# Performance work log

Measured on AMD Instinct MI355X. Metric: run time of the kernel, lower is better.

Reference implementation:

```python
import jax, jax.numpy as jnp
import numpy as np

K = 3            # kernel_size
FILTERS = 256
GC = 16          # group_channels (hardcoded in module)
G = FILTERS // GC  # groups = 16


def setup_inputs() -> dict:
    key = jax.random.key(0)
    ks = jax.random.split(key, 5)
    B, H, W, C = 8, 64, 64, FILTERS
    red = FILTERS // 4  # reduction_ratio = 4
    x = jax.random.normal(ks[0], (B, H, W, C), dtype=jnp.float32)
    W1 = jax.random.normal(ks[1], (C, red), dtype=jnp.float32) * 0.05
    b1 = jnp.zeros((red,), dtype=jnp.float32)
    W2 = jax.random.normal(ks[2], (red, K * K * G), dtype=jnp.float32) * 0.05
    b2 = jnp.zeros((K * K * G,), dtype=jnp.float32)
    return {"x": x, "W1": W1, "b1": b1, "W2": W2, "b2": b2}


def reference(x, W1, b1, W2, b2):
    b, h, w, c = x.shape
    kk = K * K
    # kernel generator: two 1x1 convs (note: norm1/relu1 are defined but unused in the original call())
    wgt = jnp.einsum('bhwc,cd->bhwd', x, W1) + b1          # [b,h,w,c/4]
    wgt = jnp.einsum('bhwd,de->bhwe', wgt, W2) + b2        # [b,h,w,kk*G]
    # transpose to channel-first, reshape (b, G, kk, h, w), expand group-channel dim
    wgt = wgt.transpose(0, 3, 1, 2).reshape(b, G, 1, kk, h, w)
    # SAME-padded 3x3 patch extraction, stride 1; TF depth layout is (ki, kj, c)
    pad = (K - 1) // 2
    xp = jnp.pad(x, ((0, 0), (pad, K - 1 - pad), (pad, K - 1 - pad), (0, 0)))
    patches = jnp.stack([xp[:, i:i + h, j:j + w, :] for i in range(K) for j in range(K)], axis=3)  # [b,h,w,kk,c]
    # replicate TF's transpose + row-major reshape of the (kk*c) flat dim into (G, GC, kk)
    out = patches.reshape(b, h, w, kk * c).transpose(0, 3, 1, 2).reshape(b, G, GC, kk, h, w)
    out = jnp.einsum('bgokhw,bgckhw->bgchw', wgt, out)     # multiply + reduce over kk
    out = out.reshape(b, FILTERS, h, w).transpose(0, 2, 3, 1)
    return out
```

## Files before the change

### kernel.cpp

```cpp
#include <hip/hip_runtime.h>

namespace {
constexpr int XP = 264;
constexpr int XR = 18 * XP;
constexpr int EWP = 148;

typedef _Float16 h2 __attribute__((ext_vector_type(2)));
typedef _Float16 h8 __attribute__((ext_vector_type(8)));
typedef float f32x4 __attribute__((ext_vector_type(4)));

__device__ __forceinline__ h2 pkrtz(float a, float b) {
  return __builtin_bit_cast(h2, __builtin_amdgcn_cvt_pkrtz(a, b));
}

#if __has_builtin(__builtin_amdgcn_fdot2)
#define HAS_FDOT2 1
#else
#define HAS_FDOT2 0
#endif

__global__ __launch_bounds__(256) void prep_w12(
    const float* __restrict__ W1, const float* __restrict__ b1,
    const float* __restrict__ W2, const float* __restrict__ b2,
    _Float16* __restrict__ pack, float* __restrict__ b12)
{
  const int t = threadIdx.x;
  const int T = blockIdx.x;
  if (T < 9) {
    __shared__ float sw2[64 * 16];
    for (int i = t; i < 1024; i += 256) {
      int d = i >> 4, n = i & 15;
      sw2[i] = W2[d * 144 + T * 16 + n];
    }
    __syncthreads();
    const int c = t;
    float acc[16];
#pragma unroll
    for (int n = 0; n < 16; ++n) acc[n] = 0.f;
    for (int d = 0; d < 64; d += 4) {
      float4 w1 = *(const float4*)(W1 + c * 64 + d);
#pragma unroll
      for (int dd = 0; dd < 4; ++dd) {
        float a = (dd == 0) ? w1.x : (dd == 1) ? w1.y : (dd == 2) ? w1.z : w1.w;
        const float* r = &sw2[(d + dd) * 16];
#pragma unroll
        for (int n = 0; n < 16; ++n) acc[n] += a * r[n];
      }
    }
    int s = c >> 5, q = (c >> 3) & 3, j = c & 7;
#pragma unroll
    for (int n = 0; n < 16; ++n)
      pack[(((T * 8 + s) * 64 + q * 16 + n) << 3) + j] = (_Float16)acc[n];
  } else if (t < 144) {
    float bb = b2[t];
    for (int d = 0; d < 64; ++d) bb += b1[d] * W2[d * 144 + t];
    b12[t] = bb;
  }
}

__global__ __launch_bounds__(256) void invo_fused(
    const float* __restrict__ x,
    const _Float16* __restrict__ pack,
    const float* __restrict__ b12g,
    float* __restrict__ out)
{
  __shared__ __align__(16) _Float16 xg[3 * XR];
  __shared__ float ew[16 * EWP];

  const int t = threadIdx.x;
  const int blk = blockIdx.x;
  const int b = blk & 7;
  const int r_ = blk >> 3;
  const int strip = r_ & 3;
  const int h = r_ >> 2;
  const int w0 = strip * 16;
  const int pix0 = ((b << 6) + h) * 64 + w0;

  for (int idx = t; idx < 3 * 18 * 64; idx += 256) {
    int c4 = (idx & 63) << 2;
    int pr = idx >> 6;
    int r = (pr >= 36) ? 2 : (pr >= 18 ? 1 : 0);
    int j = pr - r * 18;
    int hh = h + r - 1, ww = w0 + j - 1;
    float4 v = make_float4(0.f, 0.f, 0.f, 0.f);
    if (((unsigned)hh < 64u) && ((unsigned)ww < 64u))
      v = *(const float4*)(x + ((((b << 6) + hh) << 6) + ww) * 256 + c4);
    h2 lo = pkrtz(v.x, v.y), hi = pkrtz(v.z, v.w);
    uint2 u;
    u.x = __builtin_bit_cast(unsigned, lo);
    u.y = __builtin_bit_cast(unsigned, hi);
    *(uint2*)(&xg[r * XR + j * XP + c4]) = u;
  }
  __syncthreads();

  {
    const int wave = t >> 6, lane = t & 63;
    const int q = lane >> 4, m = lane & 15;
    h8 A[8];
    const _Float16* arow = &xg[XR + (m + 1) * XP + q * 8];
#pragma unroll
    for (int s = 0; s < 8; ++s)
      A[s] = *(const h8*)(arow + s * 32);
    for (int T = wave; T < 9; T += 4) {
      f32x4 acc = {0.f, 0.f, 0.f, 0.f};
      const h8* bp = (const h8*)pack + (T * 8) * 64 + lane;
#pragma unroll
      for (int s = 0; s < 8; ++s)
        acc = __builtin_amdgcn_mfma_f32_16x16x32_f16(A[s], bp[s * 64], acc, 0, 0, 0);
      float bb = b12g[T * 16 + m];
#pragma unroll
      for (int r = 0; r < 4; ++r)
        ew[(q * 4 + r) * EWP + T * 16 + m] = acc[r] + bb;
    }
  }
  __syncthreads();

  {
    const int p = t >> 4, g = t & 15;
    float ewr[9];
#pragma unroll
    for (int k = 0; k < 9; ++k) ewr[k] = ew[p * EWP + g * 9 + k];
    h2 wp[8];
#pragma unroll
    for (int m = 0; m < 8; ++m)
      wp[m] = pkrtz(ewr[m], ewr[m + 1]);
    const float w8 = ewr[8], wb0 = ewr[0];
    const int g144 = g * 144;
    const int pbase = p * XP;
    float res[16];
#pragma unroll
    for (int gc = 0; gc < 16; ++gc) res[gc] = 0.f;
#pragma unroll
    for (int j = 0; j < 18; ++j) {
      int f = g144 + j * 8;
      int tap = f >> 8;
      int ch = f & 255;
      int di = (tap * 86) >> 8;
      int dj = tap - 3 * di;
      uint4 dv = *(const uint4*)(&xg[di * XR + (p + dj) * XP + ch]);
      h2 v[4];
      v[0] = __builtin_bit_cast(h2, dv.x);
      v[1] = __builtin_bit_cast(h2, dv.y);
      v[2] = __builtin_bit_cast(h2, dv.z);
      v[3] = __builtin_bit_cast(h2, dv.w);
#pragma unroll
      for (int i = 0; i < 4; ++i) {
        const int u = j * 8 + 2 * i;
        const int m = u % 9;
        if (m == 8) {
          res[u / 9]     += (float)v[i][0] * w8;
          res[u / 9 + 1] += (float)v[i][1] * wb0;
        } else {
#if HAS_FDOT2
          res[u / 9] = __builtin_amdgcn_fdot2(v[i], wp[m], res[u / 9], false);
#else
          res[u / 9] += (float)v[i][0] * ewr[m] + (float)v[i][1] * ewr[m + 1];
#endif
        }
      }
    }
    float* orow = out + (size_t)(pix0 + p) * 256 + (g << 4);
    *(float4*)(orow + 0)  = make_float4(res[0],  res[1],  res[2],  res[3]);
    *(float4*)(orow + 4)  = make_float4(res[4],  res[5],  res[6],  res[7]);
    *(float4*)(orow + 8)  = make_float4(res[8],  res[9],  res[10], res[11]);
    *(float4*)(orow + 12) = make_float4(res[12], res[13], res[14], res[15]);
  }
}
}

extern "C" void kernel_launch(void* const* d_in, const int* in_sizes, int n_in,
                              void* d_out, int out_size, void* d_ws, size_t ws_size,
                              hipStream_t stream) {
  const float* x  = (const float*)d_in[0];
  const float* W1 = (const float*)d_in[1];
  const float* b1 = (const float*)d_in[2];
  const float* W2 = (const float*)d_in[3];
  const float* b2 = (const float*)d_in[4];
  float* out = (float*)d_out;
  _Float16* pack = (_Float16*)d_ws;
  float* b12 = (float*)((char*)d_ws + 73728);
  prep_w12<<<10, 256, 0, stream>>>(W1, b1, W2, b2, pack, b12);
  invo_fused<<<2048, 256, 0, stream>>>(x, pack, b12, out);
}
```

Measured before the change: 114.5 us.

## Pre-pack padded fp16 input slabs and load tiles via global-to-LDS DMA

Adds a prep kernel that converts x to fp16 and writes zero-padded 18-wide strip slabs into workspace. The main kernel then fills shared memory with direct global_load_lds 16-byte transfers, so it no longer needs per-element bounds checks and fp32-to-fp16 conversion in the load loop. In exchange it makes an extra full pass over x, with writes to and reads from a workspace buffer, plus an extra kernel launch. It falls back to the old kernel if the workspace is too small.

```diff
diff --git a/kernel.cpp b/kernel.cpp
--- a/kernel.cpp
+++ b/kernel.cpp
@@ -4,6 +4,7 @@
 constexpr int XP = 264;
 constexpr int XR = 18 * XP;
 constexpr int EWP = 148;
+constexpr size_t SLAB = (size_t)67 * XR;
 
 typedef _Float16 h2 __attribute__((ext_vector_type(2)));
 typedef _Float16 h8 __attribute__((ext_vector_type(8)));
@@ -11,6 +12,12 @@
 
 __device__ __forceinline__ h2 pkrtz(float a, float b) {
   return __builtin_bit_cast(h2, __builtin_amdgcn_cvt_pkrtz(a, b));
+}
+
+__device__ __forceinline__ void load_lds16(const void* g, void* l) {
+  __builtin_amdgcn_global_load_lds(
+      (const __attribute__((address_space(1))) void*)g,
+      (__attribute__((address_space(3))) void*)l, 16, 0, 0);
 }
 
 #if __has_builtin(__builtin_amdgcn_fdot2)
@@ -58,13 +65,42 @@
   }
 }
 
-__global__ __launch_bounds__(256) void invo_fused(
-    const float* __restrict__ x,
+__global__ __launch_bounds__(256) void prep_xpad(
+    const float* __restrict__ x, _Float16* __restrict__ xpad)
+{
+  const int t = threadIdx.x;
+  const int blk = blockIdx.x;
+  const int s = blk % 66;
+  const int bs = blk / 66;
+  const int b = bs >> 2, strip = bs & 3;
+  const int w0 = strip * 16;
+  const int hsrc = s - 1;
+  const bool rowok = (unsigned)hsrc < 64u;
+  _Float16* dst0 = xpad + (SLAB * bs) + (size_t)s * XR;
+  for (int idx = t; idx < 594; idx += 256) {
+    int j = idx / 33, cc = idx % 33;
+    int w = w0 + j - 1;
+    uint4 o = make_uint4(0u, 0u, 0u, 0u);
+    if (rowok && cc < 32 && (unsigned)w < 64u) {
+      const float* src = x + (((size_t)(b * 64 + hsrc) * 64 + w) << 8) + cc * 8;
+      float4 v0 = *(const float4*)(src);
+      float4 v1 = *(const float4*)(src + 4);
+      o.x = __builtin_bit_cast(unsigned, pkrtz(v0.x, v0.y));
+      o.y = __builtin_bit_cast(unsigned, pkrtz(v0.z, v0.w));
+      o.z = __builtin_bit_cast(unsigned, pkrtz(v1.x, v1.y));
+      o.w = __builtin_bit_cast(unsigned, pkrtz(v1.z, v1.w));
+    }
+    *(uint4*)(dst0 + j * XP + cc * 8) = o;
+  }
+}
+
+__global__ __launch_bounds__(256) void invo_fused_dma(
+    const _Float16* __restrict__ xpad,
     const _Float16* __restrict__ pack,
     const float* __restrict__ b12g,
     float* __restrict__ out)
 {
-  __shared__ __align__(16) _Float16 xg[3 * XR];
+  __shared__ __align__(16) _Float16 xg[1792 * 8];
   __shared__ float ew[16 * EWP];
 
   const int t = threadIdx.x;
@@ -75,7 +111,107 @@
   const int h = r_ >> 2;
   const int w0 = strip * 16;
   const int pix0 = ((b << 6) + h) * 64 + w0;
-
+  const int wave = t >> 6, lane = t & 63;
+
+  {
+    const char* gsrc = (const char*)(xpad + SLAB * (b * 4 + strip) + (size_t)h * XR);
+    char* lds = (char*)xg;
+    const int base = wave * 7168 + lane * 16;
+#pragma unroll
+    for (int i = 0; i < 7; ++i) {
+      int off = base + i * 1024;
+      load_lds16(gsrc + off, lds + off);
+    }
+  }
+  __syncthreads();
+
+  {
+    const int q = lane >> 4, m = lane & 15;
+    h8 A[8];
+    const _Float16* arow = &xg[XR + (m + 1) * XP + q * 8];
+#pragma unroll
+    for (int s = 0; s < 8; ++s)
+      A[s] = *(const h8*)(arow + s * 32);
+    for (int T = wave; T < 9; T += 4) {
+      f32x4 acc = {0.f, 0.f, 0.f, 0.f};
+      const h8* bp = (const h8*)pack + (T * 8) * 64 + lane;
+#pragma unroll
+      for (int s = 0; s < 8; ++s)
+        acc = __builtin_amdgcn_mfma_f32_16x16x32_f16(A[s], bp[s * 64], acc, 0, 0, 0);
+      float bb = b12g[T * 16 + m];
+#pragma unroll
+      for (int r = 0; r < 4; ++r)
+        ew[(q * 4 + r) * EWP + T * 16 + m] = acc[r] + bb;
+    }
+  }
+  __syncthreads();
+
+  {
+    const int p = t >> 4, g = t & 15;
+    float ewr[9];
+#pragma unroll
+    for (int k = 0; k < 9; ++k) ewr[k] = ew[p * EWP + g * 9 + k];
+    h2 wp[8];
+#pragma unroll
+    for (int m = 0; m < 8; ++m)
+      wp[m] = pkrtz(ewr[m], ewr[m + 1]);
+    const float w8 = ewr[8], wb0 = ewr[0];
+    const int g144 = g * 144;
+    const int pbase = p * XP;
+    float res[16];
+#pragma unroll
+    for (int gc = 0; gc < 16; ++gc) res[gc] = 0.f;
+#pragma unroll
+    for (int j = 0; j < 18; ++j) {
+      int f = g144 + j * 8;
+      int tap = f >> 8;
+      int ch = f & 255;
+      int di = (tap * 86) >> 8;
+      int dj = tap - 3 * di;
+      uint4 dv = *(const uint4*)(&xg[di * XR + (p + dj) * XP + ch]);
+      h2 v[4];
+      v[0] = __builtin_bit_cast(h2, dv.x);
+      v[1] = __builtin_bit_cast(h2, dv.y);
+      v[2] = __builtin_bit_cast(h2, dv.z);
+      v[3] = __builtin_bit_cast(h2, dv.w);
+#pragma unroll
+      for (int i = 0; i < 4; ++i) {
+        const int u = j * 8 + 2 * i;
+        const int m = u % 9;
+        if (m == 8) {
+          res[u / 9]     += (float)v[i][0] * w8;
+          res[u / 9 + 1] += (float)v[i][1] * wb0;
+        } else {
+#if HAS_FDOT2
+          res[u / 9] = __builtin_amdgcn_fdot2(v[i], wp[m], res[u / 9], false);
+#else
+          res[u / 9] += (float)v[i][0] * ewr[m] + (float)v[i][1] * ewr[m + 1];
+#endif
+        }
+      }
+    }
+    float* orow = out + (size_t)(pix0 + p) * 256 + (g << 4);
+    *(float4*)(orow + 0)  = make_float4(res[0],  res[1],  res[2],  res[3]);
+    *(float4*)(orow + 4)  = make_float4(res[4],  res[5],  res[6],  res[7]);
+    *(float4*)(orow + 8)  = make_float4(res[8],  res[9],  res[10], res[11]);
+    *(float4*)(orow + 12) = make_float4(res[12], res[13], res[14], res[15]);
+  }
+}
+
+__global__ __launch_bounds__(256) void invo_fused(
+    const float* __restrict__ x, const _Float16* __restrict__ pack,
+    const float* __restrict__ b12g, float* __restrict__ out)
+{
+  __shared__ __align__(16) _Float16 xg[3 * XR];
+  __shared__ float ew[16 * EWP];
+  const int t = threadIdx.x;
+  const int blk = blockIdx.x;
+  const int b = blk & 7;
+  const int r_ = blk >> 3;
+  const int strip = r_ & 3;
+  const int h = r_ >> 2;
+  const int w0 = strip * 16;
+  const int pix0 = ((b << 6) + h) * 64 + w0;
   for (int idx = t; idx < 3 * 18 * 64; idx += 256) {
     int c4 = (idx & 63) << 2;
     int pr = idx >> 6;
@@ -92,15 +228,13 @@
     *(uint2*)(&xg[r * XR + j * XP + c4]) = u;
   }
   __syncthreads();
-
   {
     const int wave = t >> 6, lane = t & 63;
     const int q = lane >> 4, m = lane & 15;
     h8 A[8];
     const _Float16* arow = &xg[XR + (m + 1) * XP + q * 8];
 #pragma unroll
-    for (int s = 0; s < 8; ++s)
-      A[s] = *(const h8*)(arow + s * 32);
+    for (int s = 0; s < 8; ++s) A[s] = *(const h8*)(arow + s * 32);
     for (int T = wave; T < 9; T += 4) {
       f32x4 acc = {0.f, 0.f, 0.f, 0.f};
       const h8* bp = (const h8*)pack + (T * 8) * 64 + lane;
@@ -114,7 +248,6 @@
     }
   }
   __syncthreads();
-
   {
     const int p = t >> 4, g = t & 15;
     float ewr[9];
@@ -122,8 +255,7 @@
     for (int k = 0; k < 9; ++k) ewr[k] = ew[p * EWP + g * 9 + k];
     h2 wp[8];
 #pragma unroll
-    for (int m = 0; m < 8; ++m)
-      wp[m] = pkrtz(ewr[m], ewr[m + 1]);
+    for (int m = 0; m < 8; ++m) wp[m] = pkrtz(ewr[m], ewr[m + 1]);
     const float w8 = ewr[8], wb0 = ewr[0];
     const int g144 = g * 144;
     const int pbase = p * XP;
@@ -179,6 +311,13 @@
   float* out = (float*)d_out;
   _Float16* pack = (_Float16*)d_ws;
   float* b12 = (float*)((char*)d_ws + 73728);
+  _Float16* xpad = (_Float16*)((char*)d_ws + 131072);
+  const size_t ENEED = 131072 + (size_t)32 * SLAB * 2;
   prep_w12<<<10, 256, 0, stream>>>(W1, b1, W2, b2, pack, b12);
-  invo_fused<<<2048, 256, 0, stream>>>(x, pack, b12, out);
-}
+  if (ws_size >= ENEED) {
+    prep_xpad<<<8 * 4 * 66, 256, 0, stream>>>(x, xpad);
+    invo_fused_dma<<<2048, 256, 0, stream>>>(xpad, pack, b12, out);
+  } else {
+    invo_fused<<<2048, 256, 0, stream>>>(x, pack, b12, out);
+  }
+}
```

New measurement: 116.9 us. +2.2%, slower.

## Widen fused involution tile to 32 pixels with 512-thread blocks

Applied to the files above, without the earlier changes.

Each block now processes a 32-pixel strip instead of 16 and runs 512 threads. This cuts the halo overhead of staging the 3-row input tile in shared memory, since the block loads 34 columns for 32 outputs rather than 18 for 16. The global loads are batched into explicit register arrays so more of them are in flight before conversion to fp16, and the first weight tile for the MFMA stage is prefetched before the barrier. In exchange, shared memory per block roughly doubles, which may reduce the number of resident blocks per CU.

```diff
diff --git a/kernel.cpp b/kernel.cpp
--- a/kernel.cpp
+++ b/kernel.cpp
@@ -2,7 +2,7 @@
 
 namespace {
 constexpr int XP = 264;
-constexpr int XR = 18 * XP;
+constexpr int XRr = 34 * XP;
 constexpr int EWP = 148;
 
 typedef _Float16 h2 __attribute__((ext_vector_type(2)));
@@ -58,50 +58,114 @@
   }
 }
 
-__global__ __launch_bounds__(256) void invo_fused(
+__global__ __launch_bounds__(512, 4) void invo_fused(
     const float* __restrict__ x,
     const _Float16* __restrict__ pack,
     const float* __restrict__ b12g,
     float* __restrict__ out)
 {
-  __shared__ __align__(16) _Float16 xg[3 * XR];
-  __shared__ float ew[16 * EWP];
+  __shared__ __align__(16) _Float16 xg[3 * XRr];
+  __shared__ float ew[32 * EWP];
 
   const int t = threadIdx.x;
   const int blk = blockIdx.x;
   const int b = blk & 7;
   const int r_ = blk >> 3;
-  const int strip = r_ & 3;
-  const int h = r_ >> 2;
-  const int w0 = strip * 16;
+  const int strip = r_ & 1;
+  const int h = r_ >> 1;
+  const int w0 = strip * 32;
   const int pix0 = ((b << 6) + h) * 64 + w0;
-
-  for (int idx = t; idx < 3 * 18 * 64; idx += 256) {
-    int c4 = (idx & 63) << 2;
-    int pr = idx >> 6;
-    int r = (pr >= 36) ? 2 : (pr >= 18 ? 1 : 0);
-    int j = pr - r * 18;
-    int hh = h + r - 1, ww = w0 + j - 1;
-    float4 v = make_float4(0.f, 0.f, 0.f, 0.f);
-    if (((unsigned)hh < 64u) && ((unsigned)ww < 64u))
-      v = *(const float4*)(x + ((((b << 6) + hh) << 6) + ww) * 256 + c4);
-    h2 lo = pkrtz(v.x, v.y), hi = pkrtz(v.z, v.w);
-    uint2 u;
-    u.x = __builtin_bit_cast(unsigned, lo);
-    u.y = __builtin_bit_cast(unsigned, hi);
-    *(uint2*)(&xg[r * XR + j * XP + c4]) = u;
+  const int wave = t >> 6, lane = t & 63;
+  const int wv = wave >> 1, ph = wave & 1;
+
+  h8 Bpre[8];
+  {
+    const h8* bp = (const h8*)pack + (wv * 8) * 64 + lane;
+#pragma unroll
+    for (int s = 0; s < 8; ++s) Bpre[s] = bp[s * 64];
+  }
+
+  {
+    float4 va[3][2];
+    int dsta[3];
+#pragma unroll
+    for (int i = 0; i < 3; ++i) {
+      int idx = i * 512 + t;
+      int cc = idx & 31, pj = idx >> 5;
+      int r = (pj >= 68) ? 2 : (pj >= 34 ? 1 : 0);
+      int j = pj - 34 * r;
+      int hh = h + r - 1, ww = w0 + j - 1;
+      dsta[i] = r * XRr + j * XP + cc * 8;
+      va[i][0] = make_float4(0.f, 0.f, 0.f, 0.f);
+      va[i][1] = make_float4(0.f, 0.f, 0.f, 0.f);
+      if (((unsigned)hh < 64u) && ((unsigned)ww < 64u)) {
+        const float* src = x + ((((b << 6) + hh) << 6) + ww) * 256 + cc * 8;
+        va[i][0] = *(const float4*)(src);
+        va[i][1] = *(const float4*)(src + 4);
+      }
+    }
+#pragma unroll
+    for (int i = 0; i < 3; ++i) {
+      uint4 o;
+      o.x = __builtin_bit_cast(unsigned, pkrtz(va[i][0].x, va[i][0].y));
+      o.y = __builtin_bit_cast(unsigned, pkrtz(va[i][0].z, va[i][0].w));
+      o.z = __builtin_bit_cast(unsigned, pkrtz(va[i][1].x, va[i][1].y));
+      o.w = __builtin_bit_cast(unsigned, pkrtz(va[i][1].z, va[i][1].w));
+      *(uint4*)(&xg[dsta[i]]) = o;
+    }
+    float4 vb[4][2];
+    int dstb[4];
+    bool okb[4];
+#pragma unroll
+    for (int i = 0; i < 4; ++i) {
+      int idx = (i + 3) * 512 + t;
+      okb[i] = idx < 3264;
+      int cc = idx & 31, pj = idx >> 5;
+      int r = (pj >= 68) ? 2 : (pj >= 34 ? 1 : 0);
+      int j = pj - 34 * r;
+      int hh = h + r - 1, ww = w0 + j - 1;
+      dstb[i] = r * XRr + j * XP + cc * 8;
+      vb[i][0] = make_float4(0.f, 0.f, 0.f, 0.f);
+      vb[i][1] = make_float4(0.f, 0.f, 0.f, 0.f);
+      if (okb[i] && ((unsigned)hh < 64u) && ((unsigned)ww < 64u)) {
+        const float* src = x + ((((b << 6) + hh) << 6) + ww) * 256 + cc * 8;
+        vb[i][0] = *(const float4*)(src);
+        vb[i][1] = *(const float4*)(src + 4);
+      }
+    }
+#pragma unroll
+    for (int i = 0; i < 4; ++i) {
+      if (okb[i]) {
+        uint4 o;
+        o.x = __builtin_bit_cast(unsigned, pkrtz(vb[i][0].x, vb[i][0].y));
+        o.y = __builtin_bit_cast(unsigned, pkrtz(vb[i][0].z, vb[i][0].w));
+        o.z = __builtin_bit_cast(unsigned, pkrtz(vb[i][1].x, vb[i][1].y));
+        o.w = __builtin_bit_cast(unsigned, pkrtz(vb[i][1].z, vb[i][1].w));
+        *(uint4*)(&xg[dstb[i]]) = o;
+      }
+    }
   }
   __syncthreads();
 
   {
-    const int wave = t >> 6, lane = t & 63;
     const int q = lane >> 4, m = lane & 15;
     h8 A[8];
-    const _Float16* arow = &xg[XR + (m + 1) * XP + q * 8];
+    const _Float16* arow = &xg[XRr + (ph * 16 + m + 1) * XP + q * 8];
 #pragma unroll
     for (int s = 0; s < 8; ++s)
       A[s] = *(const h8*)(arow + s * 32);
-    for (int T = wave; T < 9; T += 4) {
+    {
+      const int T = wv;
+      f32x4 acc = {0.f, 0.f, 0.f, 0.f};
+#pragma unroll
+      for (int s = 0; s < 8; ++s)
+        acc = __builtin_amdgcn_mfma_f32_16x16x32_f16(A[s], Bpre[s], acc, 0, 0, 0);
+      float bb = b12g[T * 16 + m];
+#pragma unroll
+      for (int r = 0; r < 4; ++r)
+        ew[(ph * 16 + q * 4 + r) * EWP + T * 16 + m] = acc[r] + bb;
+    }
+    for (int T = wv + 4; T < 9; T += 4) {
       f32x4 acc = {0.f, 0.f, 0.f, 0.f};
       const h8* bp = (const h8*)pack + (T * 8) * 64 + lane;
 #pragma unroll
@@ -110,7 +174,7 @@
       float bb = b12g[T * 16 + m];
 #pragma unroll
       for (int r = 0; r < 4; ++r)
-        ew[(q * 4 + r) * EWP + T * 16 + m] = acc[r] + bb;
+        ew[(ph * 16 + q * 4 + r) * EWP + T * 16 + m] = acc[r] + bb;
     }
   }
   __syncthreads();
@@ -136,8 +200,8 @@
       int tap = f >> 8;
       int ch = f & 255;
       int di = (tap * 86) >> 8;
-      int dj = tap - 3 * di;
-      uint4 dv = *(const uint4*)(&xg[di * XR + (p + dj) * XP + ch]);
+      int off = XP * (tap + 31 * di) + ch;
+      uint4 dv = *(const uint4*)(&xg[pbase + off]);
       h2 v[4];
       v[0] = __builtin_bit_cast(h2, dv.x);
       v[1] = __builtin_bit_cast(h2, dv.y);
@@ -180,5 +244,5 @@
   _Float16* pack = (_Float16*)d_ws;
   float* b12 = (float*)((char*)d_ws + 73728);
   prep_w12<<<10, 256, 0, stream>>>(W1, b1, W2, b2, pack, b12);
-  invo_fused<<<2048, 256, 0, stream>>>(x, pack, b12, out);
-}
+  invo_fused<<<1024, 512, 0, stream>>>(x, pack, b12, out);
+}
```

After: 110.1 us. 3.8% less time.
